# Optimization experiments

Hardware: AMD Instinct MI355X
Metric: run time of the kernel (lower is better)

## Reference

```python
import jax, jax.numpy as jnp
import numpy as np

B, S, D = 2, 2048, 2048
H = 16
HD = D // H
SCALE = 1.0 / (HD ** 0.5)


def setup_inputs() -> dict:
    key = jax.random.key(0)
    ks = jax.random.split(key, 9)
    std = 0.02
    return {
        "x": jax.random.normal(ks[0], (B, S, D), dtype=jnp.float32),
        "q_w": jax.random.normal(ks[1], (D, D), dtype=jnp.float32) * std,
        "q_b": jax.random.normal(ks[2], (D,), dtype=jnp.float32) * std,
        "k_w": jax.random.normal(ks[3], (D, D), dtype=jnp.float32) * std,
        "k_b": jax.random.normal(ks[4], (D,), dtype=jnp.float32) * std,
        "v_w": jax.random.normal(ks[5], (D, D), dtype=jnp.float32) * std,
        "v_b": jax.random.normal(ks[6], (D,), dtype=jnp.float32) * std,
        "o_w": jax.random.normal(ks[7], (D, D), dtype=jnp.float32) * std,
        "o_b": jax.random.normal(ks[8], (D,), dtype=jnp.float32) * std,
    }


def reference(x, q_w, q_b, k_w, k_b, v_w, v_b, o_w, o_b):
    # torch Linear: y = x @ W.T + b  (weights stored [out, in])
    b, s, _ = x.shape
    dtype = x.dtype
    q = (x @ q_w.T + q_b).reshape(b, s, H, HD).transpose(0, 2, 1, 3)  # [B,H,S,HD]
    k = (x @ k_w.T + k_b).reshape(b, s, H, HD).transpose(0, 2, 1, 3)
    v = (x @ v_w.T + v_b).reshape(b, s, H, HD).transpose(0, 2, 1, 3)
    scores = jnp.einsum("bhqd,bhkd->bhqk", q, k) * SCALE  # [B,H,S,S]
    # causal mask: positions k > q get -inf (via triu(diagonal=1))
    causal = jnp.triu(jnp.ones((s, s), dtype=bool), k=1)
    scores = jnp.where(causal[None, None], -jnp.inf, scores)
    attn = jax.nn.softmax(scores.astype(jnp.float32), axis=-1).astype(dtype)
    out = jnp.einsum("bhqk,bhkd->bhqd", attn, v)  # [B,H,S,HD]
    out = out.transpose(0, 2, 1, 3).reshape(b, s, H * HD)
    return out @ o_w.T + o_b
```

## Files before the change

### kernel.cpp

```cpp
#include <hip/hip_runtime.h>
#include <hip/hip_bf16.h>

#define S_LEN 2048
#define DMODEL 2048
#define NH 16
#define HDIM 128
#define SCALE_F 0.08838834764831845f

typedef __attribute__((ext_vector_type(8))) short bf16x8;
typedef __attribute__((ext_vector_type(4))) float f32x4;

__device__ __forceinline__ unsigned short f2bf(float f) {
  unsigned int u = __float_as_uint(f);
  u += 0x7FFFu + ((u >> 16) & 1u);
  return (unsigned short)(u >> 16);
}

__device__ __forceinline__ void gload16(const void* g, void* l) {
  __builtin_amdgcn_global_load_lds(
      (const __attribute__((address_space(1))) unsigned int*)g,
      (__attribute__((address_space(3))) unsigned int*)l, 16, 0, 0);
}

__global__ __launch_bounds__(256) void cvt_all(
    const float* __restrict__ x, const float* __restrict__ qw,
    const float* __restrict__ kw, const float* __restrict__ vw,
    const float* __restrict__ ow, unsigned short* __restrict__ xb,
    unsigned short* __restrict__ wqkv, unsigned short* __restrict__ wo) {
  int i = blockIdx.x * blockDim.x + threadIdx.x;
  const float* src;
  unsigned short* dst;
  int off;
  if (i < 2097152) {
    src = x; dst = xb; off = i;
  } else {
    const int j = i - 2097152;
    const int wsel = j >> 20;
    off = j & 1048575;
    src = (wsel == 0) ? qw : (wsel == 1) ? kw : (wsel == 2) ? vw : ow;
    dst = (wsel == 0) ? wqkv
        : (wsel == 1) ? (wqkv + 4194304)
        : (wsel == 2) ? (wqkv + 8388608)
                      : wo;
  }
  const float4 v = *(const float4*)(src + (size_t)off * 4);
  ushort4 o;
  o.x = f2bf(v.x); o.y = f2bf(v.y); o.z = f2bf(v.z); o.w = f2bf(v.w);
  *(ushort4*)(dst + (size_t)off * 4) = o;
}

__device__ __forceinline__ void gemm_core_128x256(
    const unsigned short* __restrict__ Ag, const unsigned short* __restrict__ Wg,
    int m0, int n0, char* lds, int t, f32x4 (&acc)[4][4]) {
  const int lane = t & 63, w = t >> 6;
  const int wr = w >> 2, wc = w & 3;

#pragma unroll
  for (int mi = 0; mi < 4; ++mi)
#pragma unroll
    for (int nj = 0; nj < 4; ++nj)
#pragma unroll
      for (int e = 0; e < 4; ++e) acc[mi][nj][e] = 0.f;

  const int fr = lane & 15;
  const int sw16 = (((lane >> 4) ^ ((lane >> 1) & 3)) << 4);
  const int aRowBase = (wr * 64 + fr) * 64;
  const int bRowBase = (wc * 64 + fr) * 64;

  const int cg8 = (((t & 3) ^ ((t >> 3) & 3)) * 8);
  const unsigned short* sAbase = Ag + (m0 + (t >> 2)) * DMODEL + cg8;
  const unsigned short* sBbase0 = Wg + (n0 + (t >> 2)) * DMODEL + cg8;
  const unsigned short* sBbase1 = sBbase0 + 128 * DMODEL;
  char* dstW = lds + w * 1024;

  auto stage3 = [&](int Tc, int h, int buf) {
    const int koff = Tc * 64 + h * 32;
    gload16(sAbase + koff, dstW + buf * 16384 + h * 8192);
    gload16(sBbase0 + koff, dstW + 49152 + buf * 32768 + h * 16384);
    gload16(sBbase1 + koff, dstW + 49152 + buf * 32768 + h * 16384 + 8192);
  };

  auto phase = [&](int h, int bufR, int doStage, int TS, int bufS, int vm) {
    const int rA = bufR * 16384 + h * 8192;
    const int rB = 49152 + bufR * 32768 + h * 16384;
    bf16x8 a[4], b[4];
#pragma unroll
    for (int mi = 0; mi < 4; ++mi)
      a[mi] = *(const bf16x8*)(lds + rA + aRowBase + mi * 1024 + sw16);
#pragma unroll
    for (int nj = 0; nj < 4; ++nj)
      b[nj] = *(const bf16x8*)(lds + rB + bRowBase + nj * 1024 + sw16);
    if (doStage) stage3(TS, h, bufS);
    if (vm == 6) asm volatile("s_waitcnt vmcnt(6)" ::: "memory");
    if (vm == 0) asm volatile("s_waitcnt vmcnt(0)" ::: "memory");
    __builtin_amdgcn_s_barrier();
    __builtin_amdgcn_s_setprio(1);
#pragma unroll
    for (int mi = 0; mi < 4; ++mi)
#pragma unroll
      for (int nj = 0; nj < 4; ++nj)
        acc[mi][nj] = __builtin_amdgcn_mfma_f32_16x16x32_bf16(
            a[mi], b[nj], acc[mi][nj], 0, 0, 0);
    __builtin_amdgcn_s_setprio(0);
    __builtin_amdgcn_s_barrier();
  };

  stage3(0, 0, 0);
  stage3(0, 1, 0);
  stage3(1, 0, 1);
  stage3(1, 1, 1);
  asm volatile("s_waitcnt vmcnt(6)" ::: "memory");
  __builtin_amdgcn_s_barrier();

#pragma unroll 1
  for (int k3 = 0; k3 < 10; ++k3) {
    const int T = k3 * 3;
    phase(0, 0, 1, T + 2, 2, -1);
    phase(1, 0, 1, T + 2, 2, 6);
    phase(0, 1, 1, T + 3, 0, -1);
    phase(1, 1, 1, T + 3, 0, 6);
    phase(0, 2, 1, T + 4, 1, -1);
    phase(1, 2, 1, T + 4, 1, 6);
  }
  phase(0, 0, 0, 0, 0, -1);
  phase(1, 0, 0, 0, 0, 0);
  phase(0, 1, 0, 0, 0, -1);
  phase(1, 1, 0, 0, 0, -1);
}

__global__ __launch_bounds__(512, 1) void gemm_qkv(
    const unsigned short* __restrict__ A, const unsigned short* __restrict__ W,
    const float* __restrict__ qbias, const float* __restrict__ kbias,
    const float* __restrict__ vbias,
    unsigned short* __restrict__ qo, unsigned short* __restrict__ ko,
    unsigned short* __restrict__ vto) {
  extern __shared__ char lds[];
  const int t = threadIdx.x;
  const int swz = ((int)blockIdx.x & 7) * 96 + ((int)blockIdx.x >> 3);
  const int m0 = (swz & 31) * 128;
  const int n0 = (swz >> 5) * 256;

  f32x4 acc[4][4];
  gemm_core_128x256(A, W, m0, n0, lds, t, acc);

  const int lane = t & 63, w = t >> 6;
  const int wr = w >> 2, wc = w & 3;
  const int b_ = m0 >> 11;
  const int proj = n0 >> 11;
  const int nn_base = (n0 & 2047) + wc * 64;
  const float* bias = (proj == 0) ? qbias : ((proj == 1) ? kbias : vbias);

  if (proj == 2) {
    unsigned short* Tv = (unsigned short*)lds;
#pragma unroll
    for (int nj = 0; nj < 4; ++nj) {
      const int col = wc * 64 + nj * 16 + (lane & 15);
      const float bv = bias[nn_base - wc * 64 + col - (nj * 16 + (lane & 15)) +
                            nj * 16 + (lane & 15)];
#pragma unroll
      for (int mi = 0; mi < 4; ++mi) {
        const int row0 = wr * 64 + mi * 16 + (lane >> 4) * 4;
        ushort4 pk;
        pk.x = f2bf(acc[mi][nj][0] + bv);
        pk.y = f2bf(acc[mi][nj][1] + bv);
        pk.z = f2bf(acc[mi][nj][2] + bv);
        pk.w = f2bf(acc[mi][nj][3] + bv);
        *(ushort4*)&Tv[col * 136 + row0] = pk;
      }
    }
    __syncthreads();
    const int col = t >> 1, half = t & 1;
    const int nn = (n0 & 2047) + col;
    const int h = nn >> 7, hd = nn & 127;
    unsigned short* base =
        vto + (size_t)((b_ * NH + h) * HDIM + hd) * S_LEN + (m0 & 2047) +
        half * 64;
#pragma unroll
    for (int u = 0; u < 8; ++u)
      *(bf16x8*)(base + u * 8) =
          *(const bf16x8*)&Tv[col * 136 + half * 64 + u * 8];
  } else {
    unsigned short* Tq = (unsigned short*)lds;
#pragma unroll
    for (int nj = 0; nj < 4; ++nj) {
      const int col = wc * 64 + nj * 16 + (lane & 15);
      const float bv = bias[(n0 & 2047) + col];
#pragma unroll
      for (int mi = 0; mi < 4; ++mi) {
        const int row0 = wr * 64 + mi * 16 + (lane >> 4) * 4;
#pragma unroll
        for (int r = 0; r < 4; ++r)
          Tq[(row0 + r) * 264 + col] = f2bf(acc[mi][nj][r] + bv);
      }
    }
    __syncthreads();
    const int lr = t >> 2, qc = t & 3;
    const int s = (m0 & 2047) + lr;
    unsigned short* qk = (proj == 0) ? qo : ko;
#pragma unroll
    for (int u = 0; u < 8; ++u) {
      const int lc = qc * 64 + u * 8;
      const int nn = (n0 & 2047) + lc;
      const int h = nn >> 7, hd = nn & 127;
      *(bf16x8*)(qk + (size_t)((b_ * NH + h) * S_LEN + s) * HDIM + hd) =
          *(const bf16x8*)&Tq[lr * 264 + lc];
    }
  }
}

__global__ __launch_bounds__(512, 1) void gemm_out(
    const unsigned short* __restrict__ A, const unsigned short* __restrict__ W,
    const float* __restrict__ bias, float* __restrict__ out) {
  extern __shared__ char lds[];
  const int t = threadIdx.x;
  const int swz = ((int)blockIdx.x & 7) * 32 + ((int)blockIdx.x >> 3);
  const int m0 = (swz & 31) * 128;
  const int n0 = (swz >> 5) * 256;

  f32x4 acc[4][4];
  gemm_core_128x256(A, W, m0, n0, lds, t, acc);

  const int lane = t & 63, w = t >> 6;
  const int wr = w >> 2, wc = w & 3;
#pragma unroll
  for (int nj = 0; nj < 4; ++nj) {
    const int n = n0 + wc * 64 + nj * 16 + (lane & 15);
    const float bv = bias[n];
#pragma unroll
    for (int mi = 0; mi < 4; ++mi) {
      const int mrow = m0 + wr * 64 + mi * 16 + (lane >> 4) * 4;
      float* dst = out + (size_t)mrow * DMODEL + n;
#pragma unroll
      for (int r = 0; r < 4; r++) dst[r * DMODEL] = acc[mi][nj][r] + bv;
    }
  }
}

__global__ __launch_bounds__(256, 2) void attn_fwd(
    const unsigned short* __restrict__ Q,
    const unsigned short* __restrict__ K,
    const unsigned short* __restrict__ VT,
    unsigned short* __restrict__ ctx) {
  __shared__ unsigned short Ks[2][64 * 128];
  __shared__ unsigned short Vs[2][128 * 64];
  __shared__ unsigned short Ps[4][16 * 64];
  const int t = threadIdx.x, lane = t & 63, w = t >> 6;
  const int bid = blockIdx.x;
  const int bh = ((bid & 7) << 2) + ((bid >> 3) & 3);
  const int xq = bid >> 5;
  const unsigned short* Qb = Q + bh * (S_LEN * HDIM);
  const unsigned short* Kb = K + bh * (S_LEN * HDIM);
  const unsigned short* Vb = VT + bh * (HDIM * S_LEN);
  const int b_ = bh >> 4, h = bh & 15;

  auto stageKV = [&](int buf, int kv0) {
#pragma unroll
    for (int u = 0; u < 4; ++u) {
      const int c = t + u * 256;
      const int row = c >> 4, cc = c & 15;
      gload16(Kb + (kv0 + row) * HDIM + ((cc ^ (row & 7)) * 8),
              (char*)Ks[buf] + u * 4096 + w * 1024);
    }
#pragma unroll
    for (int u = 0; u < 4; ++u) {
      const int c = t + u * 256;
      const int row = c >> 3, cc = c & 7;
      gload16(Vb + row * S_LEN + kv0 + ((cc ^ (row & 7)) * 8),
              (char*)Vs[buf] + u * 4096 + w * 1024);
    }
  };

#pragma unroll 1
  for (int pi = 0; pi < 2; ++pi) {
    const int qtile = pi ? (31 - xq) : xq;
    const int q0 = qtile * 64 + w * 16;

    bf16x8 qf[4];
    {
      const unsigned short* qrow =
          Qb + (q0 + (lane & 15)) * HDIM + (lane >> 4) * 8;
#pragma unroll
      for (int dk = 0; dk < 4; dk++) qf[dk] = *(const bf16x8*)(qrow + dk * 32);
    }

    float mrow[4], lrow[4];
    f32x4 oacc[8];
#pragma unroll
    for (int r = 0; r < 4; r++) { mrow[r] = -__builtin_inff(); lrow[r] = 0.f; }
#pragma unroll
    for (int d = 0; d < 8; d++)
#pragma unroll
      for (int e = 0; e < 4; e++) oacc[d][e] = 0.f;

    const int nt = qtile + 1;
    stageKV(0, 0);
    __syncthreads();
    int cur = 0;

#pragma unroll 1
    for (int kt = 0; kt < nt; ++kt) {
      if (kt + 1 < nt) stageKV(cur ^ 1, (kt + 1) * 64);

      const unsigned short* Kc = Ks[cur];
      const unsigned short* Vc = Vs[cur];
      const int kv0 = kt * 64;

      f32x4 sacc[4];
#pragma unroll
      for (int ck = 0; ck < 4; ck++)
#pragma unroll
        for (int e = 0; e < 4; e++) sacc[ck][e] = 0.f;
      __builtin_amdgcn_s_setprio(1);
#pragma unroll
      for (int ck = 0; ck < 4; ++ck) {
        const int krow = ck * 16 + (lane & 15);
#pragma unroll
        for (int dk = 0; dk < 4; ++dk) {
          const int chunk = dk * 4 + (lane >> 4);
          const bf16x8 kf = *(const bf16x8*)((const char*)Kc + krow * 256 +
                                             ((chunk ^ (krow & 7)) << 4));
          sacc[ck] = __builtin_amdgcn_mfma_f32_16x16x32_bf16(qf[dk], kf,
                                                             sacc[ck], 0, 0, 0);
        }
      }
      __builtin_amdgcn_s_setprio(0);
#pragma unroll
      for (int ck = 0; ck < 4; ck++)
#pragma unroll
        for (int r = 0; r < 4; r++) sacc[ck][r] *= SCALE_F;
      if (kt == qtile) {
#pragma unroll
        for (int ck = 0; ck < 4; ck++) {
          const int col = kv0 + ck * 16 + (lane & 15);
#pragma unroll
          for (int r = 0; r < 4; r++) {
            const int rowq = q0 + (lane >> 4) * 4 + r;
            if (col > rowq) sacc[ck][r] = -__builtin_inff();
          }
        }
      }
      float tmax[4];
#pragma unroll
      for (int r = 0; r < 4; r++)
        tmax[r] = fmaxf(fmaxf(sacc[0][r], sacc[1][r]),
                        fmaxf(sacc[2][r], sacc[3][r]));
#pragma unroll
      for (int off = 1; off < 16; off <<= 1)
#pragma unroll
        for (int r = 0; r < 4; r++)
          tmax[r] = fmaxf(tmax[r], __shfl_xor(tmax[r], off, 64));
      bool need = false;
#pragma unroll
      for (int r = 0; r < 4; r++) need |= (tmax[r] > mrow[r] + 8.f);
      if (__any(need)) {
#pragma unroll
        for (int r = 0; r < 4; r++) {
          const float mn = fmaxf(mrow[r], tmax[r]);
          const float corr = __expf(mrow[r] - mn);
          mrow[r] = mn;
          lrow[r] *= corr;
#pragma unroll
          for (int d = 0; d < 8; d++) oacc[d][r] *= corr;
        }
      }
#pragma unroll
      for (int ck = 0; ck < 4; ck++)
#pragma unroll
        for (int r = 0; r < 4; r++) {
          const float p = __expf(sacc[ck][r] - mrow[r]);
          lrow[r] += p;
          const int prow = (lane >> 4) * 4 + r;
          const int pcol = ck * 16 + (lane & 15);
          *(unsigned short*)((char*)Ps[w] +
                             ((prow * 128 + pcol * 2) ^ ((prow & 7) << 4))) =
              f2bf(p);
        }

      bf16x8 pf[2];
      {
        const int prow = lane & 15;
#pragma unroll
        for (int kk = 0; kk < 2; kk++) {
          const int chunk = kk * 4 + (lane >> 4);
          pf[kk] = *(const bf16x8*)((const char*)Ps[w] + prow * 128 +
                                    ((chunk ^ (prow & 7)) << 4));
        }
      }
      __builtin_amdgcn_s_setprio(1);
#pragma unroll
      for (int d = 0; d < 8; ++d) {
        const int vrow = d * 16 + (lane & 15);
#pragma unroll
        for (int kk = 0; kk < 2; ++kk) {
          const int chunk = kk * 4 + (lane >> 4);
          const bf16x8 vf = *(const bf16x8*)((const char*)Vc + vrow * 128 +
                                             ((chunk ^ (vrow & 7)) << 4));
          oacc[d] = __builtin_amdgcn_mfma_f32_16x16x32_bf16(pf[kk], vf, oacc[d],
                                                            0, 0, 0);
        }
      }
      __builtin_amdgcn_s_setprio(0);

      __syncthreads();
      cur ^= 1;
    }

#pragma unroll
    for (int off = 1; off < 16; off <<= 1)
#pragma unroll
      for (int r = 0; r < 4; r++) lrow[r] += __shfl_xor(lrow[r], off, 64);
#pragma unroll
    for (int r = 0; r < 4; r++) {
      const float inv = 1.f / lrow[r];
      const int srow = q0 + (lane >> 4) * 4 + r;
      unsigned short* dst =
          ctx + (b_ * S_LEN + srow) * DMODEL + h * HDIM + (lane & 15);
#pragma unroll
      for (int d = 0; d < 8; d++) dst[d * 16] = f2bf(oacc[d][r] * inv);
    }
  }
}

extern "C" void kernel_launch(void* const* d_in, const int* in_sizes, int n_in,
                              void* d_out, int out_size, void* d_ws,
                              size_t ws_size, hipStream_t stream) {
  const float* x  = (const float*)d_in[0];
  const float* qw = (const float*)d_in[1];
  const float* qb = (const float*)d_in[2];
  const float* kw = (const float*)d_in[3];
  const float* kb = (const float*)d_in[4];
  const float* vw = (const float*)d_in[5];
  const float* vb = (const float*)d_in[6];
  const float* ow = (const float*)d_in[7];
  const float* ob = (const float*)d_in[8];
  float* out = (float*)d_out;

  unsigned short* xb   = (unsigned short*)d_ws;
  unsigned short* wqkv = xb + (size_t)8388608;
  unsigned short* wo   = wqkv + (size_t)12582912;
  unsigned short* qt_  = wo + (size_t)4194304;
  unsigned short* kt_  = qt_ + (size_t)8388608;
  unsigned short* vt_  = kt_ + (size_t)8388608;
  unsigned short* ctx  = vt_ + (size_t)8388608;

  cvt_all<<<24576, 256, 0, stream>>>(x, qw, kw, vw, ow, xb, wqkv, wo);

  gemm_qkv<<<768, 512, 147456, stream>>>(xb, wqkv, qb, kb, vb, qt_, kt_, vt_);
  attn_fwd<<<512, 256, 0, stream>>>(qt_, kt_, vt_, ctx);
  gemm_out<<<256, 512, 147456, stream>>>(ctx, wo, ob, out);
}
```

Baseline: 266.5 us.

## Use 128-row query tiles with 8 warps in attention; drop LDS transpose for Q/K

Attention now runs 512-thread blocks covering 128 query rows, so each staged K/V tile feeds twice as many query rows and the total K/V load traffic drops. The grid halves to 256 blocks with one block per CU, and the causal mask check becomes per-warp. Separately, the Q/K epilogue of the QKV GEMM writes bf16 values directly to global memory instead of staging them through LDS for vectorized stores. That removes a barrier but replaces the wide stores with scattered 2-byte writes, and the new attention layout risks lower occupancy and extra masked work in the diagonal tiles.

```diff
diff --git a/kernel.cpp b/kernel.cpp
--- a/kernel.cpp
+++ b/kernel.cpp
@@ -147,7 +147,6 @@
   const int wr = w >> 2, wc = w & 3;
   const int b_ = m0 >> 11;
   const int proj = n0 >> 11;
-  const int nn_base = (n0 & 2047) + wc * 64;
   const float* bias = (proj == 0) ? qbias : ((proj == 1) ? kbias : vbias);
 
   if (proj == 2) {
@@ -155,8 +154,7 @@
 #pragma unroll
     for (int nj = 0; nj < 4; ++nj) {
       const int col = wc * 64 + nj * 16 + (lane & 15);
-      const float bv = bias[nn_base - wc * 64 + col - (nj * 16 + (lane & 15)) +
-                            nj * 16 + (lane & 15)];
+      const float bv = bias[(n0 & 2047) + col];
 #pragma unroll
       for (int mi = 0; mi < 4; ++mi) {
         const int row0 = wr * 64 + mi * 16 + (lane >> 4) * 4;
@@ -180,30 +178,21 @@
       *(bf16x8*)(base + u * 8) =
           *(const bf16x8*)&Tv[col * 136 + half * 64 + u * 8];
   } else {
-    unsigned short* Tq = (unsigned short*)lds;
+    const int nn_base = (n0 & 2047) + wc * 64;
 #pragma unroll
     for (int nj = 0; nj < 4; ++nj) {
-      const int col = wc * 64 + nj * 16 + (lane & 15);
-      const float bv = bias[(n0 & 2047) + col];
+      const int nn = nn_base + nj * 16 + (lane & 15);
+      const int h = nn >> 7, hd = nn & 127;
+      const float bv = bias[nn];
 #pragma unroll
       for (int mi = 0; mi < 4; ++mi) {
-        const int row0 = wr * 64 + mi * 16 + (lane >> 4) * 4;
-#pragma unroll
-        for (int r = 0; r < 4; ++r)
-          Tq[(row0 + r) * 264 + col] = f2bf(acc[mi][nj][r] + bv);
-      }
-    }
-    __syncthreads();
-    const int lr = t >> 2, qc = t & 3;
-    const int s = (m0 & 2047) + lr;
-    unsigned short* qk = (proj == 0) ? qo : ko;
-#pragma unroll
-    for (int u = 0; u < 8; ++u) {
-      const int lc = qc * 64 + u * 8;
-      const int nn = (n0 & 2047) + lc;
-      const int h = nn >> 7, hd = nn & 127;
-      *(bf16x8*)(qk + (size_t)((b_ * NH + h) * S_LEN + s) * HDIM + hd) =
-          *(const bf16x8*)&Tq[lr * 264 + lc];
+        const int mrow = m0 + wr * 64 + mi * 16 + (lane >> 4) * 4;
+        const int s = mrow & 2047;
+        unsigned short* dst =
+            ((proj == 0) ? qo : ko) + ((b_ * NH + h) * S_LEN + s) * HDIM + hd;
+#pragma unroll
+        for (int r = 0; r < 4; r++) dst[r * HDIM] = f2bf(acc[mi][nj][r] + bv);
+      }
     }
   }
 }
@@ -236,18 +225,18 @@
   }
 }
 
-__global__ __launch_bounds__(256, 2) void attn_fwd(
+__global__ __launch_bounds__(512, 1) void attn_fwd(
     const unsigned short* __restrict__ Q,
     const unsigned short* __restrict__ K,
     const unsigned short* __restrict__ VT,
     unsigned short* __restrict__ ctx) {
   __shared__ unsigned short Ks[2][64 * 128];
   __shared__ unsigned short Vs[2][128 * 64];
-  __shared__ unsigned short Ps[4][16 * 64];
+  __shared__ unsigned short Ps[8][16 * 64];
   const int t = threadIdx.x, lane = t & 63, w = t >> 6;
   const int bid = blockIdx.x;
   const int bh = ((bid & 7) << 2) + ((bid >> 3) & 3);
-  const int xq = bid >> 5;
+  const int xp = bid >> 5;
   const unsigned short* Qb = Q + bh * (S_LEN * HDIM);
   const unsigned short* Kb = K + bh * (S_LEN * HDIM);
   const unsigned short* Vb = VT + bh * (HDIM * S_LEN);
@@ -255,25 +244,25 @@
 
   auto stageKV = [&](int buf, int kv0) {
 #pragma unroll
-    for (int u = 0; u < 4; ++u) {
-      const int c = t + u * 256;
+    for (int u = 0; u < 2; ++u) {
+      const int c = t + u * 512;
       const int row = c >> 4, cc = c & 15;
       gload16(Kb + (kv0 + row) * HDIM + ((cc ^ (row & 7)) * 8),
-              (char*)Ks[buf] + u * 4096 + w * 1024);
-    }
-#pragma unroll
-    for (int u = 0; u < 4; ++u) {
-      const int c = t + u * 256;
+              (char*)Ks[buf] + u * 8192 + w * 1024);
+    }
+#pragma unroll
+    for (int u = 0; u < 2; ++u) {
+      const int c = t + u * 512;
       const int row = c >> 3, cc = c & 7;
       gload16(Vb + row * S_LEN + kv0 + ((cc ^ (row & 7)) * 8),
-              (char*)Vs[buf] + u * 4096 + w * 1024);
+              (char*)Vs[buf] + u * 8192 + w * 1024);
     }
   };
 
 #pragma unroll 1
   for (int pi = 0; pi < 2; ++pi) {
-    const int qtile = pi ? (31 - xq) : xq;
-    const int q0 = qtile * 64 + w * 16;
+    const int qtile = pi ? (15 - xp) : xp;
+    const int q0 = qtile * 128 + w * 16;
 
     bf16x8 qf[4];
     {
@@ -292,7 +281,7 @@
 #pragma unroll
       for (int e = 0; e < 4; e++) oacc[d][e] = 0.f;
 
-    const int nt = qtile + 1;
+    const int nt = 2 * qtile + 2;
     stageKV(0, 0);
     __syncthreads();
     int cur = 0;
@@ -328,7 +317,7 @@
       for (int ck = 0; ck < 4; ck++)
 #pragma unroll
         for (int r = 0; r < 4; r++) sacc[ck][r] *= SCALE_F;
-      if (kt == qtile) {
+      if (kv0 + 63 > q0) {
 #pragma unroll
         for (int ck = 0; ck < 4; ck++) {
           const int col = kv0 + ck * 16 + (lane & 15);
@@ -446,6 +435,6 @@
   cvt_all<<<24576, 256, 0, stream>>>(x, qw, kw, vw, ow, xb, wqkv, wo);
 
   gemm_qkv<<<768, 512, 147456, stream>>>(xb, wqkv, qb, kb, vb, qt_, kt_, vt_);
-  attn_fwd<<<512, 256, 0, stream>>>(qt_, kt_, vt_, ctx);
+  attn_fwd<<<256, 512, 0, stream>>>(qt_, kt_, vt_, ctx);
   gemm_out<<<256, 512, 147456, stream>>>(ctx, wo, ob, out);
 }
```

Result: no change. 269.3 us (+1.1%).
